# Performance work log

Measured on AMD Instinct MI355X. Metric: run time of the kernel, lower is better.

The kernel has to match this reference:

```python
import jax, jax.numpy as jnp
import numpy as np

B, T, D, H = 8, 4096, 1024, 1024


def setup_inputs() -> dict:
    key = jax.random.key(0)
    ks = jax.random.split(key, 8)
    s = 1.0 / np.sqrt(D)
    x = jax.random.normal(ks[0], (B, T, D), dtype=jnp.float32)
    Wq = jax.random.uniform(ks[1], (H, D), jnp.float32, -s, s)
    bq = jax.random.uniform(ks[2], (H,), jnp.float32, -s, s)
    Wk = jax.random.uniform(ks[3], (H, D), jnp.float32, -s, s)
    bk = jax.random.uniform(ks[4], (H,), jnp.float32, -s, s)
    Wv = jax.random.uniform(ks[5], (H, D), jnp.float32, -s, s)
    bv = jax.random.uniform(ks[6], (H,), jnp.float32, -s, s)
    wbias = jax.random.uniform(ks[7], (H,), jnp.float32, 0.0, 1.0)  # torch.rand
    return {"x": x, "Wq": Wq, "bq": bq, "Wk": Wk, "bk": bk, "Wv": Wv, "bv": bv, "wbias": wbias}


def reference(x, Wq, bq, Wk, bk, Wv, bv, wbias):
    # Q, K, V: [B, T, H]
    Q = jnp.einsum('btd,hd->bth', x, Wq) + bq
    K = jnp.einsum('btd,hd->bth', x, Wk) + bk
    V = jnp.einsum('btd,hd->bth', x, Wv) + bv
    Q_sig = jax.nn.sigmoid(Q)
    numer = jnp.exp(K + wbias)            # [B, T, H]
    denom = numer.sum(axis=0)             # [T, H] (faithful: sum over batch axis)
    weighted = (numer * V).sum(axis=0) / denom  # [T, H]
    Yt = Q_sig * weighted                 # broadcast -> [B, T, H]
    return Yt  # to_out is Identity since dim == hidden_dim
```

## Files before the change

### kernel.cpp

```cpp
#include <hip/hip_runtime.h>
#include <hip/hip_bf16.h>

#define B_ 8
#define T_ 4096
#define D_ 1024
#define H_ 1024

typedef __attribute__((ext_vector_type(8))) short short8;
typedef __attribute__((ext_vector_type(4))) float floatx4;

#define GLOAD16(gptr, lptr) \
  __builtin_amdgcn_global_load_lds((const __attribute__((address_space(1))) void*)(gptr), \
                                   (__attribute__((address_space(3))) void*)(lptr), 16, 0, 0)

__device__ __forceinline__ ushort f2b(float f) {
  unsigned x = __builtin_bit_cast(unsigned, f);
  unsigned r = (x + 0x7fffu + ((x >> 16) & 1u)) >> 16;
  return (ushort)r;
}

__global__ void cvt_kernel(const float* __restrict__ in, ushort* __restrict__ out, int n) {
  int idx = blockIdx.x * blockDim.x + threadIdx.x;
  int stride = gridDim.x * blockDim.x;
  for (long i = (long)idx * 8; i < n; i += (long)stride * 8) {
    const float4 f0 = *(const float4*)(in + i);
    const float4 f1 = *(const float4*)(in + i + 4);
    union { ushort u[8]; uint4 v; } r;
    r.u[0] = f2b(f0.x); r.u[1] = f2b(f0.y); r.u[2] = f2b(f0.z); r.u[3] = f2b(f0.w);
    r.u[4] = f2b(f1.x); r.u[5] = f2b(f1.y); r.u[6] = f2b(f1.z); r.u[7] = f2b(f1.w);
    *(uint4*)(out + i) = r.v;
  }
}

__global__ __launch_bounds__(256, 2) void kv_kernel(
    const ushort* __restrict__ xb, const ushort* __restrict__ Wkb,
    const ushort* __restrict__ Wvb, const float* __restrict__ bk,
    const float* __restrict__ bv, const float* __restrict__ wbias,
    float* __restrict__ weighted) {
  __shared__ ushort As[2][128 * 64];
  __shared__ ushort Ks[2][64 * 64];
  __shared__ ushort Vs[2][64 * 64];

  const int tid = threadIdx.x;
  const int lane = tid & 63;
  const int w = tid >> 6;
  const int wrow = w >> 1;
  const int wcol = w & 1;
  const int t0 = blockIdx.x * 128;
  const int h0 = blockIdx.y * 64;

  const int sr = tid >> 3;
  const int swz = (tid & 7) ^ ((tid >> 3) & 7);

  const int arow = wrow * 64 + (lane & 15);
  const int bcol = wcol * 32 + (lane & 15);
  const int cs0 = ((lane >> 4) + 0) ^ (lane & 7);
  const int cs1 = ((lane >> 4) + 4) ^ (lane & 7);

  float wbc[2], bkc[2], bvc[2];
#pragma unroll
  for (int n = 0; n < 2; ++n) {
    int h = h0 + wcol * 32 + n * 16 + (lane & 15);
    wbc[n] = wbias[h];
    bkc[n] = bk[h];
    bvc[n] = bv[h];
  }

  const ushort* ksb = Wkb + (size_t)h0 * D_ + (size_t)sr * D_ + swz * 8;
  const ushort* vsb = Wvb + (size_t)h0 * D_ + (size_t)sr * D_ + swz * 8;
  const ushort* xsb = xb + (size_t)t0 * D_ + (size_t)sr * D_ + swz * 8;

  auto stage = [&](int p, int nb) {
    const int b = p >> 4;
    const int kt = (p & 15) << 6;
    const ushort* xs = xsb + (size_t)b * (T_ * D_) + kt;
#pragma unroll
    for (int it = 0; it < 4; ++it)
      GLOAD16(xs + (size_t)(it * 32) * D_, &As[nb][(it * 256 + tid) * 8]);
#pragma unroll
    for (int it = 0; it < 2; ++it) {
      GLOAD16(ksb + kt + (size_t)(it * 32) * D_, &Ks[nb][(it * 256 + tid) * 8]);
      GLOAD16(vsb + kt + (size_t)(it * 32) * D_, &Vs[nb][(it * 256 + tid) * 8]);
    }
  };

  floatx4 accK[4][2] = {};
  floatx4 accV[4][2] = {};
  floatx4 sumN[4][2] = {};
  floatx4 sumWV[4][2] = {};

  stage(0, 0);
  __syncthreads();

  for (int p = 0; p < 128; ++p) {
    const int cur = p & 1;
    if (p + 1 < 128) stage(p + 1, cur ^ 1);

#pragma unroll
    for (int s = 0; s < 2; ++s) {
      const int cs = s ? cs1 : cs0;
      short8 a[4], kb[2], vb[2];
#pragma unroll
      for (int m = 0; m < 4; ++m)
        a[m] = *(const short8*)&As[cur][(arow + m * 16) * 64 + cs * 8];
#pragma unroll
      for (int n = 0; n < 2; ++n) {
        kb[n] = *(const short8*)&Ks[cur][(bcol + n * 16) * 64 + cs * 8];
        vb[n] = *(const short8*)&Vs[cur][(bcol + n * 16) * 64 + cs * 8];
      }
#pragma unroll
      for (int m = 0; m < 4; ++m)
#pragma unroll
        for (int n = 0; n < 2; ++n) {
          accK[m][n] = __builtin_amdgcn_mfma_f32_16x16x32_bf16(a[m], kb[n], accK[m][n], 0, 0, 0);
          accV[m][n] = __builtin_amdgcn_mfma_f32_16x16x32_bf16(a[m], vb[n], accV[m][n], 0, 0, 0);
        }
    }

    if ((p & 15) == 15) {
#pragma unroll
      for (int m = 0; m < 4; ++m)
#pragma unroll
        for (int n = 0; n < 2; ++n) {
#pragma unroll
          for (int r = 0; r < 4; ++r) {
            float nmr = __expf(accK[m][n][r] + bkc[n] + wbc[n]);
            sumN[m][n][r] += nmr;
            sumWV[m][n][r] += nmr * (accV[m][n][r] + bvc[n]);
          }
          accK[m][n] = floatx4{0.f, 0.f, 0.f, 0.f};
          accV[m][n] = floatx4{0.f, 0.f, 0.f, 0.f};
        }
    }
    __syncthreads();
  }

#pragma unroll
  for (int m = 0; m < 4; ++m)
#pragma unroll
    for (int n = 0; n < 2; ++n)
#pragma unroll
      for (int r = 0; r < 4; ++r) {
        int t = t0 + wrow * 64 + m * 16 + (lane >> 4) * 4 + r;
        int h = h0 + wcol * 32 + n * 16 + (lane & 15);
        weighted[(size_t)t * H_ + h] = sumWV[m][n][r] / sumN[m][n][r];
      }
}

__global__ __launch_bounds__(256, 3) void q_kernel(
    const ushort* __restrict__ xb, const ushort* __restrict__ Wqb,
    const float* __restrict__ bq, const float* __restrict__ weighted,
    float* __restrict__ out) {
  __shared__ ushort As[2][128 * 32];
  __shared__ ushort Bs[2][128 * 32];

  const int tid = threadIdx.x;
  const int lane = tid & 63;
  const int w = tid >> 6;
  const int wrow = w >> 1;
  const int wcol = w & 1;
  const int R0 = blockIdx.x * 128;
  const int h0 = blockIdx.y * 128;

  const int srow = tid >> 2;
  const int sq = (tid & 3) ^ ((tid >> 3) & 3);

  const int arow = wrow * 64 + (lane & 15);
  const int brow = wcol * 64 + (lane & 15);
  const int cq = (lane >> 4) ^ ((lane >> 1) & 3);

  const ushort* xsrc = xb + ((size_t)R0 + srow) * D_ + sq * 8;
  const ushort* wsrc = Wqb + ((size_t)h0 + srow) * D_ + sq * 8;

  auto stage = [&](int kt, int buf) {
    GLOAD16(xsrc + kt, &As[buf][tid * 8]);
    GLOAD16(xsrc + (size_t)64 * D_ + kt, &As[buf][(tid + 256) * 8]);
    GLOAD16(wsrc + kt, &Bs[buf][tid * 8]);
    GLOAD16(wsrc + (size_t)64 * D_ + kt, &Bs[buf][(tid + 256) * 8]);
  };

  floatx4 acc[4][4] = {};

  stage(0, 0);
  __syncthreads();

  for (int it = 0; it < D_ / 32; ++it) {
    const int cur = it & 1;
    if (it + 1 < D_ / 32) stage((it + 1) * 32, cur ^ 1);

    short8 a[4], bb[4];
#pragma unroll
    for (int m = 0; m < 4; ++m)
      a[m] = *(const short8*)&As[cur][(arow + m * 16) * 32 + cq * 8];
#pragma unroll
    for (int n = 0; n < 4; ++n)
      bb[n] = *(const short8*)&Bs[cur][(brow + n * 16) * 32 + cq * 8];
#pragma unroll
    for (int m = 0; m < 4; ++m)
#pragma unroll
      for (int n = 0; n < 4; ++n)
        acc[m][n] = __builtin_amdgcn_mfma_f32_16x16x32_bf16(a[m], bb[n], acc[m][n], 0, 0, 0);
    __syncthreads();
  }

  float bqc[4];
#pragma unroll
  for (int n = 0; n < 4; ++n)
    bqc[n] = bq[h0 + wcol * 64 + n * 16 + (lane & 15)];

#pragma unroll
  for (int m = 0; m < 4; ++m)
#pragma unroll
    for (int n = 0; n < 4; ++n)
#pragma unroll
      for (int r = 0; r < 4; ++r) {
        int row = R0 + wrow * 64 + m * 16 + (lane >> 4) * 4 + r;
        int t = row & (T_ - 1);
        int h = h0 + wcol * 64 + n * 16 + (lane & 15);
        float q = acc[m][n][r] + bqc[n];
        float sig = 1.f / (1.f + __expf(-q));
        out[(size_t)row * H_ + h] = sig * weighted[(size_t)t * H_ + h];
      }
}

extern "C" void kernel_launch(void* const* d_in, const int* in_sizes, int n_in,
                              void* d_out, int out_size, void* d_ws, size_t ws_size,
                              hipStream_t stream) {
  (void)in_sizes; (void)n_in; (void)out_size; (void)ws_size;
  const float* x = (const float*)d_in[0];
  const float* Wq = (const float*)d_in[1];
  const float* bq = (const float*)d_in[2];
  const float* Wk = (const float*)d_in[3];
  const float* bk = (const float*)d_in[4];
  const float* Wv = (const float*)d_in[5];
  const float* bv = (const float*)d_in[6];
  const float* wbias = (const float*)d_in[7];
  float* out = (float*)d_out;

  char* ws = (char*)d_ws;
  const size_t XN = (size_t)B_ * T_ * D_;
  const size_t WN = (size_t)H_ * D_;
  ushort* xb  = (ushort*)ws;
  ushort* Wqb = (ushort*)(ws + XN * 2);
  ushort* Wkb = Wqb + WN;
  ushort* Wvb = Wkb + WN;
  float* weighted = (float*)(ws + XN * 2 + 3 * WN * 2);

  cvt_kernel<<<2048, 256, 0, stream>>>(x, xb, (int)XN);
  cvt_kernel<<<512, 256, 0, stream>>>(Wq, Wqb, (int)WN);
  cvt_kernel<<<512, 256, 0, stream>>>(Wk, Wkb, (int)WN);
  cvt_kernel<<<512, 256, 0, stream>>>(Wv, Wvb, (int)WN);

  kv_kernel<<<dim3(T_ / 128, H_ / 64), 256, 0, stream>>>(xb, Wkb, Wvb, bk, bv, wbias, weighted);
  q_kernel<<<dim3((B_ * T_) / 128, H_ / 128), 256, 0, stream>>>(xb, Wqb, bq, weighted, out);
}
```

Measured before the change: 296.0 us.

## Triple-buffer LDS pipelines with 512-thread blocks and larger row tiles

Both GEMM kernels now run 512-thread blocks covering twice as many rows, which raises reuse of the weight tiles. The double-buffered __syncthreads loop becomes a three-stage pipeline in dynamic LDS: loads run two stages ahead, fenced by explicit vmcnt waits and a single s_barrier per iteration. The MFMA sections are also wrapped in s_setprio so compute waves win issue slots. The cost is much larger LDS footprints (144KB for kv, 72KB for q), which limits blocks per CU.

```diff
diff --git a/kernel.cpp b/kernel.cpp
--- a/kernel.cpp
+++ b/kernel.cpp
@@ -32,29 +32,30 @@
   }
 }
 
-__global__ __launch_bounds__(256, 2) void kv_kernel(
+__global__ __launch_bounds__(512, 2) void kv_kernel(
     const ushort* __restrict__ xb, const ushort* __restrict__ Wkb,
     const ushort* __restrict__ Wvb, const float* __restrict__ bk,
     const float* __restrict__ bv, const float* __restrict__ wbias,
     float* __restrict__ weighted) {
-  __shared__ ushort As[2][128 * 64];
-  __shared__ ushort Ks[2][64 * 64];
-  __shared__ ushort Vs[2][64 * 64];
+  extern __shared__ ushort lds[];
+  ushort* const AsB = lds;
+  ushort* const KsB = lds + 49152;
+  ushort* const VsB = lds + 61440;
 
   const int tid = threadIdx.x;
   const int lane = tid & 63;
   const int w = tid >> 6;
   const int wrow = w >> 1;
   const int wcol = w & 1;
-  const int t0 = blockIdx.x * 128;
+  const int t0 = blockIdx.x * 256;
   const int h0 = blockIdx.y * 64;
 
-  const int sr = tid >> 3;
+  const int srow = tid >> 3;
   const int swz = (tid & 7) ^ ((tid >> 3) & 7);
 
   const int arow = wrow * 64 + (lane & 15);
   const int bcol = wcol * 32 + (lane & 15);
-  const int cs0 = ((lane >> 4) + 0) ^ (lane & 7);
+  const int cs0 = (lane >> 4) ^ (lane & 7);
   const int cs1 = ((lane >> 4) + 4) ^ (lane & 7);
 
   float wbc[2], bkc[2], bvc[2];
@@ -66,22 +67,20 @@
     bvc[n] = bv[h];
   }
 
-  const ushort* ksb = Wkb + (size_t)h0 * D_ + (size_t)sr * D_ + swz * 8;
-  const ushort* vsb = Wvb + (size_t)h0 * D_ + (size_t)sr * D_ + swz * 8;
-  const ushort* xsb = xb + (size_t)t0 * D_ + (size_t)sr * D_ + swz * 8;
+  const ushort* xsb = xb + (size_t)(t0 + srow) * D_ + swz * 8;
+  const ushort* ksb = Wkb + (size_t)(h0 + srow) * D_ + swz * 8;
+  const ushort* vsb = Wvb + (size_t)(h0 + srow) * D_ + swz * 8;
 
   auto stage = [&](int p, int nb) {
     const int b = p >> 4;
     const int kt = (p & 15) << 6;
     const ushort* xs = xsb + (size_t)b * (T_ * D_) + kt;
+    ushort* Ab = AsB + nb * 16384;
 #pragma unroll
     for (int it = 0; it < 4; ++it)
-      GLOAD16(xs + (size_t)(it * 32) * D_, &As[nb][(it * 256 + tid) * 8]);
-#pragma unroll
-    for (int it = 0; it < 2; ++it) {
-      GLOAD16(ksb + kt + (size_t)(it * 32) * D_, &Ks[nb][(it * 256 + tid) * 8]);
-      GLOAD16(vsb + kt + (size_t)(it * 32) * D_, &Vs[nb][(it * 256 + tid) * 8]);
-    }
+      GLOAD16(xs + (size_t)(it * 64) * D_, Ab + (it * 512 + tid) * 8);
+    GLOAD16(ksb + kt, KsB + nb * 4096 + tid * 8);
+    GLOAD16(vsb + kt, VsB + nb * 4096 + tid * 8);
   };
 
   floatx4 accK[4][2] = {};
@@ -90,31 +89,38 @@
   floatx4 sumWV[4][2] = {};
 
   stage(0, 0);
-  __syncthreads();
-
+  stage(1, 1);
+  asm volatile("s_waitcnt vmcnt(6)" ::: "memory");
+  __builtin_amdgcn_s_barrier();
+
+  int cur = 0, stg = 2;
   for (int p = 0; p < 128; ++p) {
-    const int cur = p & 1;
-    if (p + 1 < 128) stage(p + 1, cur ^ 1);
-
+    if (p < 126) stage(p + 2, stg);
+
+    const ushort* Ac = AsB + cur * 16384;
+    const ushort* Kc = KsB + cur * 4096;
+    const ushort* Vc = VsB + cur * 4096;
 #pragma unroll
     for (int s = 0; s < 2; ++s) {
       const int cs = s ? cs1 : cs0;
-      short8 a[4], kb[2], vb[2];
+      short8 a[4], kb2[2], vb2[2];
 #pragma unroll
       for (int m = 0; m < 4; ++m)
-        a[m] = *(const short8*)&As[cur][(arow + m * 16) * 64 + cs * 8];
+        a[m] = *(const short8*)&Ac[(arow + m * 16) * 64 + cs * 8];
 #pragma unroll
       for (int n = 0; n < 2; ++n) {
-        kb[n] = *(const short8*)&Ks[cur][(bcol + n * 16) * 64 + cs * 8];
-        vb[n] = *(const short8*)&Vs[cur][(bcol + n * 16) * 64 + cs * 8];
+        kb2[n] = *(const short8*)&Kc[(bcol + n * 16) * 64 + cs * 8];
+        vb2[n] = *(const short8*)&Vc[(bcol + n * 16) * 64 + cs * 8];
       }
+      __builtin_amdgcn_s_setprio(1);
 #pragma unroll
       for (int m = 0; m < 4; ++m)
 #pragma unroll
         for (int n = 0; n < 2; ++n) {
-          accK[m][n] = __builtin_amdgcn_mfma_f32_16x16x32_bf16(a[m], kb[n], accK[m][n], 0, 0, 0);
-          accV[m][n] = __builtin_amdgcn_mfma_f32_16x16x32_bf16(a[m], vb[n], accV[m][n], 0, 0, 0);
+          accK[m][n] = __builtin_amdgcn_mfma_f32_16x16x32_bf16(a[m], kb2[n], accK[m][n], 0, 0, 0);
+          accV[m][n] = __builtin_amdgcn_mfma_f32_16x16x32_bf16(a[m], vb2[n], accV[m][n], 0, 0, 0);
         }
+      __builtin_amdgcn_s_setprio(0);
     }
 
     if ((p & 15) == 15) {
@@ -132,7 +138,12 @@
           accV[m][n] = floatx4{0.f, 0.f, 0.f, 0.f};
         }
     }
-    __syncthreads();
+
+    if (p < 126) { asm volatile("s_waitcnt vmcnt(6)" ::: "memory"); }
+    else         { asm volatile("s_waitcnt vmcnt(0)" ::: "memory"); }
+    __builtin_amdgcn_s_barrier();
+    cur = (cur == 2) ? 0 : cur + 1;
+    stg = (stg == 2) ? 0 : stg + 1;
   }
 
 #pragma unroll
@@ -147,19 +158,20 @@
       }
 }
 
-__global__ __launch_bounds__(256, 3) void q_kernel(
+__global__ __launch_bounds__(512, 2) void q_kernel(
     const ushort* __restrict__ xb, const ushort* __restrict__ Wqb,
     const float* __restrict__ bq, const float* __restrict__ weighted,
     float* __restrict__ out) {
-  __shared__ ushort As[2][128 * 32];
-  __shared__ ushort Bs[2][128 * 32];
+  extern __shared__ ushort lds[];
+  ushort* const AsB = lds;
+  ushort* const BsB = lds + 24576;
 
   const int tid = threadIdx.x;
   const int lane = tid & 63;
   const int w = tid >> 6;
   const int wrow = w >> 1;
   const int wcol = w & 1;
-  const int R0 = blockIdx.x * 128;
+  const int R0 = blockIdx.x * 256;
   const int h0 = blockIdx.y * 128;
 
   const int srow = tid >> 2;
@@ -167,40 +179,50 @@
 
   const int arow = wrow * 64 + (lane & 15);
   const int brow = wcol * 64 + (lane & 15);
-  const int cq = (lane >> 4) ^ ((lane >> 1) & 3);
-
-  const ushort* xsrc = xb + ((size_t)R0 + srow) * D_ + sq * 8;
-  const ushort* wsrc = Wqb + ((size_t)h0 + srow) * D_ + sq * 8;
-
-  auto stage = [&](int kt, int buf) {
-    GLOAD16(xsrc + kt, &As[buf][tid * 8]);
-    GLOAD16(xsrc + (size_t)64 * D_ + kt, &As[buf][(tid + 256) * 8]);
-    GLOAD16(wsrc + kt, &Bs[buf][tid * 8]);
-    GLOAD16(wsrc + (size_t)64 * D_ + kt, &Bs[buf][(tid + 256) * 8]);
+  const int cq = (lane >> 4) ^ (((lane & 15) >> 1) & 3);
+
+  const ushort* xsrc = xb + (size_t)(R0 + srow) * D_ + sq * 8;
+  const ushort* wsrc = Wqb + (size_t)(h0 + srow) * D_ + sq * 8;
+
+  auto stage = [&](int kt, int nb) {
+    GLOAD16(xsrc + kt, AsB + nb * 8192 + tid * 8);
+    GLOAD16(xsrc + (size_t)128 * D_ + kt, AsB + nb * 8192 + (tid + 512) * 8);
+    GLOAD16(wsrc + kt, BsB + nb * 4096 + tid * 8);
   };
 
   floatx4 acc[4][4] = {};
 
   stage(0, 0);
-  __syncthreads();
-
-  for (int it = 0; it < D_ / 32; ++it) {
-    const int cur = it & 1;
-    if (it + 1 < D_ / 32) stage((it + 1) * 32, cur ^ 1);
-
+  stage(32, 1);
+  asm volatile("s_waitcnt vmcnt(3)" ::: "memory");
+  __builtin_amdgcn_s_barrier();
+
+  int cur = 0, stg = 2;
+  for (int it = 0; it < 32; ++it) {
+    if (it < 30) stage((it + 2) * 32, stg);
+
+    const ushort* Ac = AsB + cur * 8192;
+    const ushort* Bc = BsB + cur * 4096;
     short8 a[4], bb[4];
 #pragma unroll
     for (int m = 0; m < 4; ++m)
-      a[m] = *(const short8*)&As[cur][(arow + m * 16) * 32 + cq * 8];
+      a[m] = *(const short8*)&Ac[(arow + m * 16) * 32 + cq * 8];
 #pragma unroll
     for (int n = 0; n < 4; ++n)
-      bb[n] = *(const short8*)&Bs[cur][(brow + n * 16) * 32 + cq * 8];
+      bb[n] = *(const short8*)&Bc[(brow + n * 16) * 32 + cq * 8];
+    __builtin_amdgcn_s_setprio(1);
 #pragma unroll
     for (int m = 0; m < 4; ++m)
 #pragma unroll
       for (int n = 0; n < 4; ++n)
         acc[m][n] = __builtin_amdgcn_mfma_f32_16x16x32_bf16(a[m], bb[n], acc[m][n], 0, 0, 0);
-    __syncthreads();
+    __builtin_amdgcn_s_setprio(0);
+
+    if (it < 30) { asm volatile("s_waitcnt vmcnt(3)" ::: "memory"); }
+    else         { asm volatile("s_waitcnt vmcnt(0)" ::: "memory"); }
+    __builtin_amdgcn_s_barrier();
+    cur = (cur == 2) ? 0 : cur + 1;
+    stg = (stg == 2) ? 0 : stg + 1;
   }
 
   float bqc[4];
@@ -246,11 +268,16 @@
   ushort* Wvb = Wkb + WN;
   float* weighted = (float*)(ws + XN * 2 + 3 * WN * 2);
 
+  (void)hipFuncSetAttribute((const void*)kv_kernel,
+                            hipFuncAttributeMaxDynamicSharedMemorySize, 147456);
+  (void)hipFuncSetAttribute((const void*)q_kernel,
+                            hipFuncAttributeMaxDynamicSharedMemorySize, 73728);
+
   cvt_kernel<<<2048, 256, 0, stream>>>(x, xb, (int)XN);
   cvt_kernel<<<512, 256, 0, stream>>>(Wq, Wqb, (int)WN);
   cvt_kernel<<<512, 256, 0, stream>>>(Wk, Wkb, (int)WN);
   cvt_kernel<<<512, 256, 0, stream>>>(Wv, Wvb, (int)WN);
 
-  kv_kernel<<<dim3(T_ / 128, H_ / 64), 256, 0, stream>>>(xb, Wkb, Wvb, bk, bv, wbias, weighted);
-  q_kernel<<<dim3((B_ * T_) / 128, H_ / 128), 256, 0, stream>>>(xb, Wqb, bq, weighted, out);
-}
+  kv_kernel<<<dim3(T_ / 256, H_ / 64), 512, 147456, stream>>>(xb, Wkb, Wvb, bk, bv, wbias, weighted);
+  q_kernel<<<dim3((B_ * T_) / 256, H_ / 128), 512, 73728, stream>>>(xb, Wqb, bq, weighted, out);
+}
```

Measured after the change: 285.0 us. -3.7%, faster.
